# Kernel tuning notes

Hardware: AMD Instinct MI355X
Metric: run time of the kernel (lower is better)

## Reference

```python
import jax, jax.numpy as jnp
import numpy as np

B, N, IN_DIM, DIM = 16, 512, 2048, 512
K, DEPTH, HEADS, DH, MLP, NC = 4, 2, 8, 64, 512, 10
INNER = HEADS * DH  # 512
TOPK = 2
TEMP = 1.0


def setup_inputs() -> dict:
    key = jax.random.key(0)
    ks = jax.random.split(key, 16)
    g = lambda i, shape, s=0.02: jax.random.normal(ks[i], shape, dtype=jnp.float32) * s
    z = lambda shape: jnp.zeros(shape, jnp.float32)
    o = lambda shape: jnp.ones(shape, jnp.float32)
    return {
        "x": jax.random.normal(ks[0], (B, N, IN_DIM), dtype=jnp.float32),
        "proj_w": g(1, (IN_DIM, DIM)),
        "proj_b": z((DIM,)),
        "qkv_w": g(2, (K, DEPTH, DIM, 3 * INNER)),
        "ao_w": g(3, (K, DEPTH, INNER, DIM)),
        "ao_b": z((K, DEPTH, DIM)),
        "ln1_g": o((K, DEPTH, DIM)),
        "ln1_b": z((K, DEPTH, DIM)),
        "ln2_g": o((K, DEPTH, DIM)),
        "ln2_b": z((K, DEPTH, DIM)),
        "mlp_w1": g(4, (K, DEPTH, DIM, MLP)),
        "mlp_b1": z((K, DEPTH, MLP)),
        "mlp_w2": g(5, (K, DEPTH, MLP, DIM)),
        "mlp_b2": z((K, DEPTH, DIM)),
        "lnf_g": o((K, DIM)),
        "lnf_b": z((K, DIM)),
        "router_w1": g(6, (DIM, 256)),
        "router_b1": z((256,)),
        "router_w2": g(7, (256, K)),
        "router_b2": z((K,)),
        "head_w1": g(8, (DIM, 128)),
        "head_b1": z((128,)),
        "head_w2": g(9, (128, NC)),
        "head_b2": z((NC,)),
    }


def _ln(x, g, b):
    m = x.mean(-1, keepdims=True)
    v = jnp.mean((x - m) ** 2, axis=-1, keepdims=True)
    return (x - m) * jax.lax.rsqrt(v + 1e-5) * g + b


def _expert(h, qkv_w, ao_w, ao_b, ln1g, ln1b, ln2g, ln2b, w1, b1, w2, b2, lnfg, lnfb):
    # h: [B, N, DIM]; pre-norm transformer, depth=DEPTH, then final LN + mean-pool.
    Bb, Nn, _ = h.shape
    scale = DH ** -0.5
    for l in range(DEPTH):
        y = _ln(h, ln1g[l], ln1b[l])
        q, k, v = jnp.split(y @ qkv_w[l], 3, axis=-1)
        q = q.reshape(Bb, Nn, HEADS, DH)
        k = k.reshape(Bb, Nn, HEADS, DH)
        v = v.reshape(Bb, Nn, HEADS, DH)
        att = jax.nn.softmax(jnp.einsum('bqhd,bkhd->bhqk', q, k) * scale, axis=-1)
        o = jnp.einsum('bhqk,bkhd->bqhd', att, v).reshape(Bb, Nn, INNER)
        h = h + o @ ao_w[l] + ao_b[l]
        y2 = _ln(h, ln2g[l], ln2b[l])
        h = h + jax.nn.gelu(y2 @ w1[l] + b1[l]) @ w2[l] + b2[l]
    return _ln(h, lnfg, lnfb).mean(1)  # [B, DIM]


def reference(x, proj_w, proj_b, qkv_w, ao_w, ao_b, ln1_g, ln1_b, ln2_g, ln2_b,
              mlp_w1, mlp_b1, mlp_w2, mlp_b2, lnf_g, lnf_b,
              router_w1, router_b1, router_w2, router_b2,
              head_w1, head_b1, head_w2, head_b2):
    # Shared projection (mode='shared')
    H = x @ proj_w + proj_b                       # [B, N, DIM]
    bag = H.mean(1)                               # [B, DIM]
    rl = jax.nn.relu(bag @ router_w1 + router_b1) @ router_w2 + router_b2
    g_soft = jax.nn.softmax(rl / TEMP, axis=-1)   # [B, K]
    vals, idx = jax.lax.top_k(g_soft, TOPK)
    w = vals / (vals.sum(-1, keepdims=True) + 1e-8)
    # Dense combine weights: [B, K], zero for non-selected experts.
    Wfull = (jax.nn.one_hot(idx, K, dtype=H.dtype) * w[..., None]).sum(1)
    latents = jnp.stack([
        _expert(H, qkv_w[e], ao_w[e], ao_b[e], ln1_g[e], ln1_b[e], ln2_g[e], ln2_b[e],
                mlp_w1[e], mlp_b1[e], mlp_w2[e], mlp_b2[e], lnf_g[e], lnf_b[e])
        for e in range(K)
    ])                                            # [K, B, DIM]
    z = jnp.einsum('kbd,bk->bd', latents, Wfull)  # weighted combine
    logits = jax.nn.relu(z @ head_w1 + head_b1) @ head_w2 + head_b2
    return (z, logits, g_soft)
```

## Files before the change

kernel.cpp:

```cpp
#include <hip/hip_runtime.h>
#include <math.h>

typedef unsigned short u16;
typedef unsigned int u32;
typedef float f32x4 __attribute__((ext_vector_type(4)));
typedef unsigned short u16x8 __attribute__((ext_vector_type(8)));
typedef unsigned short u16x4 __attribute__((ext_vector_type(4)));
typedef _Float16 f16x8 __attribute__((ext_vector_type(8)));

#define DEV static __device__ __forceinline__

constexpr int BB = 16, NN = 512, DIM = 512, DEP = 2;
constexpr long ROWS = (long)BB * NN;

DEV u16 f2h(float f){ _Float16 h = (_Float16)f; return __builtin_bit_cast(u16, h); }
DEV float h2f(u16 u){ return (float)__builtin_bit_cast(_Float16, u); }
DEV f32x4 mfma16h(u16x8 a, u16x8 b, f32x4 c){
  return __builtin_amdgcn_mfma_f32_16x16x32_f16(__builtin_bit_cast(f16x8, a), __builtin_bit_cast(f16x8, b), c, 0, 0, 0);
}
DEV u32 pkrtz(float a, float b){ auto r = __builtin_amdgcn_cvt_pkrtz(a, b); return __builtin_bit_cast(u32, r); }
DEV float gelu_f(float x){ return 0.5f * x * (1.f + tanhf(0.79788456080286536f * (x + 0.044715f * x * x * x))); }

DEV void gload16(const u16* g, u16* l){
  __builtin_amdgcn_global_load_lds((const __attribute__((address_space(1))) unsigned int*)(const void*)g,
                                   (__attribute__((address_space(3))) unsigned int*)(void*)l, 16, 0, 0);
}

DEV f32x4 vaddv(f32x4 a, f32x4 b){ f32x4 r; r[0]=a[0]+b[0]; r[1]=a[1]+b[1]; r[2]=a[2]+b[2]; r[3]=a[3]+b[3]; return r; }
DEV f32x4 shfl4(f32x4 v, int m){ f32x4 r; r[0]=__shfl_xor(v[0],m); r[1]=__shfl_xor(v[1],m); r[2]=__shfl_xor(v[2],m); r[3]=__shfl_xor(v[3],m); return r; }

__global__ __launch_bounds__(256) void castAll(const float* __restrict__ qkv_w, const float* __restrict__ ao_w,
                                               const float* __restrict__ mlp_w1, const float* __restrict__ mlp_w2,
                                               u16* __restrict__ WQ, u16* __restrict__ WAO,
                                               u16* __restrict__ W1t, u16* __restrict__ W2t)
{
  const int z = blockIdx.z;
  const float* src; u16* dst; int Nd;
  if (z < 8){ src = qkv_w + (long)z * 512 * 1536; dst = WQ + (long)z * 512 * 1536; Nd = 1536; }
  else {
    int m = (z - 8) >> 3, zz = (z - 8) & 7;
    src = (m == 0 ? ao_w : m == 1 ? mlp_w1 : mlp_w2) + (long)zz * 512 * 512;
    dst = (m == 0 ? WAO : m == 1 ? W1t : W2t) + (long)zz * 512 * 512;
    Nd = 512;
  }
  const int n0 = blockIdx.y * 32;
  if (n0 >= Nd) return;
  const int k0 = blockIdx.x * 32;
  __shared__ float t[32][33];
  const int r = threadIdx.x >> 5, cc = threadIdx.x & 31;
  #pragma unroll
  for (int i = 0; i < 4; i++) t[r + i * 8][cc] = src[(long)(k0 + r + i * 8) * Nd + n0 + cc];
  __syncthreads();
  #pragma unroll
  for (int i = 0; i < 4; i++) dst[(long)(n0 + r + i * 8) * 512 + k0 + cc] = f2h(t[cc][r + i * 8]);
}

__global__ __launch_bounds__(256) void castTp(const float* __restrict__ src, u16* __restrict__ dst)
{
  __shared__ float t[32][33];
  const int k0 = blockIdx.x * 32, n0 = blockIdx.y * 32;
  const int r = threadIdx.x >> 5, cc = threadIdx.x & 31;
  #pragma unroll
  for (int i = 0; i < 4; i++) t[r + i * 8][cc] = src[(long)(k0 + r + i * 8) * 512 + n0 + cc];
  __syncthreads();
  #pragma unroll
  for (int i = 0; i < 4; i++) dst[(long)(n0 + r + i * 8) * 2048 + k0 + cc] = f2h(t[cc][r + i * 8]);
}

__global__ __launch_bounds__(256) void xcast(const float* __restrict__ X, u16* __restrict__ Xf)
{
  long i0 = ((long)blockIdx.x * 256 + threadIdx.x) * 8;
  f32x4 v0 = *(const f32x4*)(X + i0), v1 = *(const f32x4*)(X + i0 + 4);
  u16x8 hh;
  hh[0] = f2h(v0[0]); hh[1] = f2h(v0[1]); hh[2] = f2h(v0[2]); hh[3] = f2h(v0[3]);
  hh[4] = f2h(v1[0]); hh[5] = f2h(v1[1]); hh[6] = f2h(v1[2]); hh[7] = f2h(v1[3]);
  *(u16x8*)(Xf + i0) = hh;
}

__global__ __launch_bounds__(256) void gemm_proj(const u16* __restrict__ Xf, const u16* __restrict__ WP,
                                                 const float* __restrict__ bias, u16* __restrict__ Hout)
{
  const int mt = blockIdx.x, nt = blockIdx.y;
  __shared__ __align__(16) u16 As[64 * 64], Bs[128 * 64];
  const int tid = threadIdx.x, lane = tid & 63, wv = tid >> 6;
  const int wm = wv >> 1, wn = wv & 1, l4 = lane >> 4, l15 = lane & 15;
  const long a0 = (long)(mt * 64) * 2048, b0 = (long)(nt * 128) * 2048;
  const int srow = tid >> 3, sslot = tid & 7;
  f32x4 zero = {0.f, 0.f, 0.f, 0.f};
  f32x4 acc[2][4];
  #pragma unroll
  for (int mi = 0; mi < 2; mi++)
    #pragma unroll
    for (int ni = 0; ni < 4; ni++) acc[mi][ni] = zero;

  for (int kt = 0; kt < 2048; kt += 64){
    #pragma unroll
    for (int p = 0; p < 2; p++){
      int r = p * 32 + srow;
      int sg = sslot ^ (r & 7);
      gload16(Xf + a0 + (long)r * 2048 + kt + sg * 8, As + p * 2048 + wv * 512);
    }
    #pragma unroll
    for (int p = 0; p < 4; p++){
      int r = p * 32 + srow;
      int sg = sslot ^ (r & 7);
      gload16(WP + b0 + (long)r * 2048 + kt + sg * 8, Bs + p * 2048 + wv * 512);
    }
    __syncthreads();
    #pragma unroll
    for (int ks = 0; ks < 2; ks++){
      u16x8 af[2], bfr[4];
      #pragma unroll
      for (int mi = 0; mi < 2; mi++){
        int ra = wm * 32 + mi * 16 + l15;
        af[mi] = *(const u16x8*)(As + ra * 64 + ((((ks << 2) | l4)) ^ (ra & 7)) * 8);
      }
      #pragma unroll
      for (int ni = 0; ni < 4; ni++){
        int rb = wn * 64 + ni * 16 + l15;
        bfr[ni] = *(const u16x8*)(Bs + rb * 64 + ((((ks << 2) | l4)) ^ (rb & 7)) * 8);
      }
      #pragma unroll
      for (int mi = 0; mi < 2; mi++)
        #pragma unroll
        for (int ni = 0; ni < 4; ni++)
          acc[mi][ni] = mfma16h(af[mi], bfr[ni], acc[mi][ni]);
    }
    __syncthreads();
  }
  #pragma unroll
  for (int mi = 0; mi < 2; mi++)
    #pragma unroll
    for (int ni = 0; ni < 4; ni++){
      const int gr0 = mt * 64 + wm * 32 + mi * 16 + l4 * 4;
      const int gc = nt * 128 + wn * 64 + ni * 16 + l15;
      float bb = bias[gc];
      #pragma unroll
      for (int i = 0; i < 4; i++) Hout[(long)(gr0 + i) * 512 + gc] = f2h(acc[mi][ni][i] + bb);
    }
}

template<int EPI>
__global__ __launch_bounds__(256) void gemm_bt(const u16* __restrict__ A, int K, long sAe,
                                               const u16* __restrict__ Bt, long sBe,
                                               const float* __restrict__ bias, int sBiasE,
                                               u16* __restrict__ Cout, long sCe, int N,
                                               const int* __restrict__ pairs,
                                               const u16* __restrict__ resin)
{
  const int pe = pairs[blockIdx.x >> 2];
  const int e = pe >> 4, bb = pe & 15;
  const int row0 = bb * 512 + (blockIdx.x & 3) * 128;
  const int nt = blockIdx.y;
  A += (long)e * sAe + (long)row0 * K;
  Bt += (long)e * sBe + (long)(nt * 128) * K;
  const float* bias_e = bias ? bias + (long)e * sBiasE : nullptr;

  __shared__ __align__(16) u16 As[128 * 64];
  __shared__ __align__(16) u16 Bs[128 * 64];
  const int tid = threadIdx.x, lane = tid & 63, wv = tid >> 6;
  const int wm = wv >> 1, wn = wv & 1, l4 = lane >> 4, l15 = lane & 15;
  const int srow = tid >> 3, sslot = tid & 7;
  f32x4 zero = {0.f, 0.f, 0.f, 0.f};
  f32x4 acc[4][4];
  #pragma unroll
  for (int mi = 0; mi < 4; mi++)
    #pragma unroll
    for (int ni = 0; ni < 4; ni++) acc[mi][ni] = zero;

  for (int kt = 0; kt < K; kt += 64){
    #pragma unroll
    for (int p = 0; p < 4; p++){
      int r = p * 32 + srow;
      int sg = sslot ^ (r & 7);
      long go = (long)r * K + kt + sg * 8;
      int lo = p * 2048 + wv * 512;
      gload16(A + go, As + lo);
      gload16(Bt + go, Bs + lo);
    }
    __syncthreads();
    #pragma unroll
    for (int ks = 0; ks < 2; ks++){
      u16x8 af[4], bfr[4];
      #pragma unroll
      for (int mi = 0; mi < 4; mi++){
        int ra = wm * 64 + mi * 16 + l15;
        af[mi] = *(const u16x8*)(As + ra * 64 + ((((ks << 2) | l4)) ^ (ra & 7)) * 8);
      }
      #pragma unroll
      for (int ni = 0; ni < 4; ni++){
        int rb = wn * 64 + ni * 16 + l15;
        bfr[ni] = *(const u16x8*)(Bs + rb * 64 + ((((ks << 2) | l4)) ^ (rb & 7)) * 8);
      }
      #pragma unroll
      for (int mi = 0; mi < 4; mi++)
        #pragma unroll
        for (int ni = 0; ni < 4; ni++)
          acc[mi][ni] = mfma16h(af[mi], bfr[ni], acc[mi][ni]);
    }
    __syncthreads();
  }

  #pragma unroll
  for (int mi = 0; mi < 4; mi++)
    #pragma unroll
    for (int ni = 0; ni < 4; ni++){
      const int gr0 = row0 + wm * 64 + mi * 16 + l4 * 4;
      const int gc = nt * 128 + wn * 64 + ni * 16 + l15;
      float bb2 = bias_e ? bias_e[gc] : 0.f;
      #pragma unroll
      for (int i = 0; i < 4; i++){
        float val = acc[mi][ni][i] + bb2;
        long idx = (long)e * sCe + (long)(gr0 + i) * N + gc;
        if (EPI == 0){
          Cout[idx] = f2h(val);
        } else if (EPI == 1){
          Cout[idx] = f2h(gelu_f(val));
        } else if (EPI == 2){
          Cout[idx] = f2h(h2f(Cout[idx]) + val);
        } else {
          Cout[idx] = f2h(h2f(resin[(long)(gr0 + i) * N + gc]) + val);
        }
      }
    }
}

__global__ __launch_bounds__(256) void attn(const u16* __restrict__ qkv, u16* __restrict__ obf, const int* __restrict__ pairs)
{
  const int pe = pairs[blockIdx.x >> 5];
  const int e = pe >> 4, b = pe & 15;
  const int r5 = blockIdx.x & 31;
  const int hh = r5 >> 2, qt = r5 & 3;
  const u16* base = qkv + ((long)e * ROWS + (long)b * NN) * 1536;

  __shared__ u16 Ks[64 * 72];
  __shared__ u16 Vts[64 * 72];
  __shared__ u16 Ps[4][32 * 72];
  __shared__ float Lq[4][32];
  const int tid = threadIdx.x, lane = tid & 63, wv = tid >> 6;
  const int l4 = lane >> 4, l15 = lane & 15;
  const int qr0 = qt * 128 + wv * 32;
  constexpr float CSC = 0.125f * 1.44269504088896340736f;

  u16x8 qf[2][2];
  #pragma unroll
  for (int mi = 0; mi < 2; mi++)
    #pragma unroll
    for (int ks = 0; ks < 2; ks++){
      u16x8 raw = *(const u16x8*)(base + (long)(qr0 + mi * 16 + l15) * 1536 + hh * 64 + ks * 32 + l4 * 8);
      #pragma unroll
      for (int j = 0; j < 8; j++) qf[mi][ks][j] = f2h(h2f(raw[j]) * CSC);
    }

  f32x4 zero = {0.f, 0.f, 0.f, 0.f};
  f32x4 o[2][4]; float lrun[2] = {0.f, 0.f};
  #pragma unroll
  for (int mi = 0; mi < 2; mi++)
    #pragma unroll
    for (int df = 0; df < 4; df++) o[mi][df] = zero;
  const int sr = tid >> 3, ss = tid & 7;

  for (int c = 0; c < 8; c++){
    const int kk0 = c * 64;
    u16x8 kv0 = *(const u16x8*)(base + (long)(kk0 + sr) * 1536 + 512 + hh * 64 + ss * 8);
    u16x8 kv1 = *(const u16x8*)(base + (long)(kk0 + sr + 32) * 1536 + 512 + hh * 64 + ss * 8);
    u16x8 vv0 = *(const u16x8*)(base + (long)(kk0 + sr) * 1536 + 1024 + hh * 64 + ss * 8);
    u16x8 vv1 = *(const u16x8*)(base + (long)(kk0 + sr + 32) * 1536 + 1024 + hh * 64 + ss * 8);
    __syncthreads();
    *(u16x8*)(Ks + sr * 72 + ss * 8) = kv0;
    *(u16x8*)(Ks + (sr + 32) * 72 + ss * 8) = kv1;
    #pragma unroll
    for (int j = 0; j < 8; j++){
      Vts[(ss * 8 + j) * 72 + sr] = vv0[j];
      Vts[(ss * 8 + j) * 72 + sr + 32] = vv1[j];
    }
    __syncthreads();

    u16x8 kf[4][2];
    #pragma unroll
    for (int n = 0; n < 4; n++)
      #pragma unroll
      for (int ks = 0; ks < 2; ks++)
        kf[n][ks] = *(const u16x8*)(Ks + (n * 16 + l15) * 72 + ks * 32 + l4 * 8);

    f32x4 sv[2][4];
    #pragma unroll
    for (int mi = 0; mi < 2; mi++)
      #pragma unroll
      for (int n = 0; n < 4; n++){
        sv[mi][n] = zero;
        sv[mi][n] = mfma16h(kf[n][0], qf[mi][0], sv[mi][n]);
        sv[mi][n] = mfma16h(kf[n][1], qf[mi][1], sv[mi][n]);
      }

    #pragma unroll
    for (int mi = 0; mi < 2; mi++){
      float lp = 0.f;
      #pragma unroll
      for (int n = 0; n < 4; n++){
        float p0 = __builtin_amdgcn_exp2f(sv[mi][n][0]);
        float p1 = __builtin_amdgcn_exp2f(sv[mi][n][1]);
        float p2 = __builtin_amdgcn_exp2f(sv[mi][n][2]);
        float p3 = __builtin_amdgcn_exp2f(sv[mi][n][3]);
        lp += (p0 + p1) + (p2 + p3);
        union { u32 w[2]; u16x4 h; } pk;
        pk.w[0] = pkrtz(p0, p1);
        pk.w[1] = pkrtz(p2, p3);
        *(u16x4*)(&Ps[wv][(mi * 16 + l15) * 72 + n * 16 + l4 * 4]) = pk.h;
      }
      lp += __shfl_xor(lp, 16);
      lp += __shfl_xor(lp, 32);
      lrun[mi] += lp;
    }

    u16x8 pf[2][2], vf[4][2];
    #pragma unroll
    for (int mi = 0; mi < 2; mi++)
      #pragma unroll
      for (int k2 = 0; k2 < 2; k2++)
        pf[mi][k2] = *(const u16x8*)(&Ps[wv][(mi * 16 + l15) * 72 + k2 * 32 + l4 * 8]);
    #pragma unroll
    for (int df = 0; df < 4; df++)
      #pragma unroll
      for (int k2 = 0; k2 < 2; k2++)
        vf[df][k2] = *(const u16x8*)(Vts + (df * 16 + l15) * 72 + k2 * 32 + l4 * 8);
    #pragma unroll
    for (int mi = 0; mi < 2; mi++)
      #pragma unroll
      for (int df = 0; df < 4; df++){
        o[mi][df] = mfma16h(pf[mi][0], vf[df][0], o[mi][df]);
        o[mi][df] = mfma16h(pf[mi][1], vf[df][1], o[mi][df]);
      }
  }

  if (l4 == 0){
    Lq[wv][l15] = lrun[0];
    Lq[wv][16 + l15] = lrun[1];
  }
  __syncthreads();
  #pragma unroll
  for (int mi = 0; mi < 2; mi++){
    f32x4 inv;
    #pragma unroll
    for (int i = 0; i < 4; i++) inv[i] = 1.f / Lq[wv][mi * 16 + l4 * 4 + i];
    #pragma unroll
    for (int df = 0; df < 4; df++)
      #pragma unroll
      for (int i = 0; i < 4; i++)
        obf[(long)e * ROWS * DIM + (long)(b * NN + qr0 + mi * 16 + l4 * 4 + i) * DIM + hh * 64 + df * 16 + l15]
          = f2h(o[mi][df][i] * inv[i]);
  }
}

__global__ __launch_bounds__(256) void ln_rows(const u16* __restrict__ hin, long sHe,
                                               const float* __restrict__ g, const float* __restrict__ bta,
                                               int sGE, u16* __restrict__ outb, const int* __restrict__ pairs)
{
  const int pe = pairs[blockIdx.x >> 9];
  const int e = pe >> 4;
  const int row = (pe & 15) * 512 + (blockIdx.x & 511);
  const u16* x = hin + (long)e * sHe + (long)row * DIM;
  const int tid = threadIdx.x, lane = tid & 63, wv = tid >> 6;
  float a0 = h2f(x[tid]), a1 = h2f(x[tid + 256]);
  float s = a0 + a1, sq = a0 * a0 + a1 * a1;
  #pragma unroll
  for (int m = 32; m >= 1; m >>= 1){ s += __shfl_xor(s, m); sq += __shfl_xor(sq, m); }
  __shared__ float red[2][4];
  if (lane == 0){ red[0][wv] = s; red[1][wv] = sq; }
  __syncthreads();
  float S = red[0][0] + red[0][1] + red[0][2] + red[0][3];
  float Q = red[1][0] + red[1][1] + red[1][2] + red[1][3];
  float mean = S * (1.f / DIM); float var = Q * (1.f / DIM) - mean * mean;
  float inv = rsqrtf(var + 1e-5f);
  const float* ge = g + (long)e * sGE; const float* be = bta + (long)e * sGE;
  u16* yo = outb + ((long)e * ROWS + row) * DIM;
  yo[tid] = f2h((a0 - mean) * inv * ge[tid] + be[tid]);
  yo[tid + 256] = f2h((a1 - mean) * inv * ge[tid + 256] + be[tid + 256]);
}

__global__ __launch_bounds__(512) void bag_partial(const u16* __restrict__ H, float* __restrict__ bagp)
{
  const int b = blockIdx.x, c = blockIdx.y;
  const int tid = threadIdx.x;
  const u16* r = H + ((long)b * 512 + c * 64) * DIM + tid;
  float s = 0.f;
  #pragma unroll 8
  for (int n = 0; n < 64; n++) s += h2f(r[n * DIM]);
  bagp[((long)c * BB + b) * DIM + tid] = s;
}

__global__ __launch_bounds__(256) void router_mm(const float* __restrict__ bagp, const float* __restrict__ rw1,
                                                 float* __restrict__ hidp)
{
  const int kc = blockIdx.x, b = blockIdx.y;
  const int tid = threadIdx.x;
  __shared__ float bs[64];
  if (tid < 64){
    int k = kc * 64 + tid;
    float s = 0.f;
    #pragma unroll
    for (int c = 0; c < 8; c++) s += bagp[((long)c * BB + b) * DIM + k];
    bs[tid] = s * (1.f / NN);
  }
  __syncthreads();
  float a = 0.f;
  #pragma unroll 8
  for (int k = 0; k < 64; k++) a += bs[k] * rw1[(long)(kc * 64 + k) * 256 + tid];
  hidp[((long)b * 8 + kc) * 256 + tid] = a;
}

__global__ __launch_bounds__(256) void router_fin(const float* __restrict__ hidp,
                                                  const float* __restrict__ rb1,
                                                  const float* __restrict__ rw2, const float* __restrict__ rb2,
                                                  float* __restrict__ gout, float* __restrict__ wexp, int* __restrict__ pairs)
{
  const int b = blockIdx.x;
  const int tid = threadIdx.x, lane = tid & 63, wv = tid >> 6;
  __shared__ f32x4 red2[4];
  float a = rb1[tid];
  #pragma unroll
  for (int kc = 0; kc < 8; kc++) a += hidp[((long)b * 8 + kc) * 256 + tid];
  float h = fmaxf(a, 0.f);
  f32x4 w4 = *(const f32x4*)(rw2 + tid * 4);
  f32x4 s = {h * w4[0], h * w4[1], h * w4[2], h * w4[3]};
  s = vaddv(s, shfl4(s, 1)); s = vaddv(s, shfl4(s, 2)); s = vaddv(s, shfl4(s, 4));
  s = vaddv(s, shfl4(s, 8)); s = vaddv(s, shfl4(s, 16)); s = vaddv(s, shfl4(s, 32));
  if (lane == 0) red2[wv] = s;
  __syncthreads();
  if (tid == 0){
    f32x4 lg = vaddv(vaddv(red2[0], red2[1]), vaddv(red2[2], red2[3]));
    float l4a[4]; float m = -3e38f;
    #pragma unroll
    for (int k = 0; k < 4; k++){ l4a[k] = lg[k] + rb2[k]; m = fmaxf(m, l4a[k]); }
    float ex[4]; float ssum2 = 0;
    #pragma unroll
    for (int k = 0; k < 4; k++){ ex[k] = expf(l4a[k] - m); ssum2 += ex[k]; }
    float gv[4];
    #pragma unroll
    for (int k = 0; k < 4; k++){ gv[k] = ex[k] / ssum2; gout[b * 4 + k] = gv[k]; }
    int i0 = 0; float v0 = gv[0];
    #pragma unroll
    for (int k = 1; k < 4; k++) if (gv[k] > v0){ v0 = gv[k]; i0 = k; }
    int i1 = -1; float v1 = -1.f;
    #pragma unroll
    for (int k = 0; k < 4; k++) if (k != i0 && gv[k] > v1){ v1 = gv[k]; i1 = k; }
    float den = v0 + v1 + 1e-8f;
    #pragma unroll
    for (int k = 0; k < 4; k++) wexp[k * BB + b] = (k == i0) ? (v0 / den) : ((k == i1) ? (v1 / den) : 0.f);
    pairs[2 * b]     = (i0 << 4) | b;
    pairs[2 * b + 1] = (i1 << 4) | b;
  }
}

__global__ __launch_bounds__(512) void lnf_pool(const u16* __restrict__ hin, const float* __restrict__ g, const float* __restrict__ bta,
                                                float* __restrict__ latents, const int* __restrict__ pairs)
{
  const int pe = pairs[blockIdx.x];
  const int e = pe >> 4, b = pe & 15;
  const int tid = threadIdx.x, lane = tid & 63, wv = tid >> 6;
  __shared__ float gs[512], bsh[512];
  gs[tid] = g[e * DIM + tid]; bsh[tid] = bta[e * DIM + tid];
  __syncthreads();
  float acc[8] = {0, 0, 0, 0, 0, 0, 0, 0};
  for (int n = wv; n < NN; n += 8){
    const u16* r = hin + ((long)e * ROWS + (long)b * NN + n) * DIM + lane * 8;
    u16x8 vh = *(const u16x8*)r;
    float v[8];
    #pragma unroll
    for (int j = 0; j < 8; j++) v[j] = h2f(vh[j]);
    float s = 0, sq = 0;
    #pragma unroll
    for (int j = 0; j < 8; j++){ s += v[j]; sq += v[j] * v[j]; }
    #pragma unroll
    for (int m = 32; m >= 1; m >>= 1){ s += __shfl_xor(s, m); sq += __shfl_xor(sq, m); }
    float mean = s * (1.f / DIM), var = sq * (1.f / DIM) - mean * mean, inv = rsqrtf(var + 1e-5f);
    #pragma unroll
    for (int j = 0; j < 8; j++) acc[j] += (v[j] - mean) * inv * gs[lane * 8 + j] + bsh[lane * 8 + j];
  }
  __shared__ float red[8][512];
  #pragma unroll
  for (int j = 0; j < 8; j++) red[wv][lane * 8 + j] = acc[j];
  __syncthreads();
  float ssum = 0;
  #pragma unroll
  for (int w = 0; w < 8; w++) ssum += red[w][tid];
  latents[((long)e * BB + b) * DIM + tid] = ssum * (1.f / NN);
}

__global__ __launch_bounds__(128) void combine_head(const float* __restrict__ latents, const float* __restrict__ wexp,
                                                    const float* __restrict__ hw1, const float* __restrict__ hb1,
                                                    const float* __restrict__ hw2, const float* __restrict__ hb2,
                                                    float* __restrict__ out)
{
  const int b = blockIdx.x;
  const int tid = threadIdx.x;
  __shared__ float zs[512];
  __shared__ float hid[128];
  float wk[4];
  #pragma unroll
  for (int k = 0; k < 4; k++) wk[k] = wexp[k * BB + b];
  #pragma unroll
  for (int i = 0; i < 4; i++){
    int c = tid + i * 128;
    float s = 0.f;
    #pragma unroll
    for (int k = 0; k < 4; k++) if (wk[k] != 0.f) s += wk[k] * latents[((long)k * BB + b) * DIM + c];
    zs[c] = s; out[b * 512 + c] = s;
  }
  __syncthreads();
  float h = hb1[tid];
  #pragma unroll 8
  for (int k2 = 0; k2 < 512; k2++) h += zs[k2] * hw1[k2 * 128 + tid];
  hid[tid] = fmaxf(h, 0.f);
  __syncthreads();
  if (tid < 10){
    float s = hb2[tid];
    #pragma unroll 16
    for (int j = 0; j < 128; j++) s += hid[j] * hw2[j * 10 + tid];
    out[8192 + b * 10 + tid] = s;
  }
}

extern "C" void kernel_launch(void* const* d_in, const int* in_sizes, int n_in,
                              void* d_out, int out_size, void* d_ws, size_t ws_size,
                              hipStream_t stream)
{
  const float* x      = (const float*)d_in[0];
  const float* proj_w = (const float*)d_in[1];
  const float* proj_b = (const float*)d_in[2];
  const float* qkv_w  = (const float*)d_in[3];
  const float* ao_w   = (const float*)d_in[4];
  const float* ao_b   = (const float*)d_in[5];
  const float* ln1_g  = (const float*)d_in[6];
  const float* ln1_b  = (const float*)d_in[7];
  const float* ln2_g  = (const float*)d_in[8];
  const float* ln2_b  = (const float*)d_in[9];
  const float* mlp_w1 = (const float*)d_in[10];
  const float* mlp_b1 = (const float*)d_in[11];
  const float* mlp_w2 = (const float*)d_in[12];
  const float* mlp_b2 = (const float*)d_in[13];
  const float* lnf_g  = (const float*)d_in[14];
  const float* lnf_b  = (const float*)d_in[15];
  const float* rw1    = (const float*)d_in[16];
  const float* rb1    = (const float*)d_in[17];
  const float* rw2    = (const float*)d_in[18];
  const float* rb2    = (const float*)d_in[19];
  const float* hw1    = (const float*)d_in[20];
  const float* hb1    = (const float*)d_in[21];
  const float* hw2    = (const float*)d_in[22];
  const float* hb2    = (const float*)d_in[23];
  float* out = (float*)d_out;

  char* base = (char*)d_ws; size_t off = 0;
  auto alloc = [&](size_t bytes) -> void* { void* p = base + off; off = (off + bytes + 255) & ~(size_t)255; return p; };

  u16* WQ   = (u16*)alloc((size_t)8 * 1536 * 512 * 2);
  u16* WAO  = (u16*)alloc((size_t)8 * 512 * 512 * 2);
  u16* W1t  = (u16*)alloc((size_t)8 * 512 * 512 * 2);
  u16* W2t  = (u16*)alloc((size_t)8 * 512 * 512 * 2);
  u16* WP   = (u16*)alloc((size_t)512 * 2048 * 2);
  u16* HF   = (u16*)alloc((size_t)ROWS * 512 * 2);
  u16* HH   = (u16*)alloc((size_t)4 * ROWS * 512 * 2);
  u16* YB   = (u16*)alloc((size_t)4 * ROWS * 512 * 2);
  u16* QKVb = (u16*)alloc((size_t)4 * ROWS * 1536 * 2);
  float* WEXP = (float*)alloc(64 * 4);
  int* PAIRS  = (int*)alloc(32 * 4);
  float* LAT  = (float*)alloc(4 * 16 * 512 * 4);
  float* BAGP = (float*)alloc((size_t)8 * 16 * 512 * 4);
  float* HIDP = (float*)alloc((size_t)16 * 8 * 256 * 4);
  u16* Y2B = QKVb;
  u16* TB  = QKVb + (size_t)4 * ROWS * 512;
  u16* OB  = YB;
  u16* Xf  = QKVb;

  castAll<<<dim3(16, 48, 32), 256, 0, stream>>>(qkv_w, ao_w, mlp_w1, mlp_w2, WQ, WAO, W1t, W2t);
  castTp<<<dim3(64, 16), 256, 0, stream>>>(proj_w, WP);
  xcast<<<8192, 256, 0, stream>>>(x, Xf);

  gemm_proj<<<dim3(128, 4), 256, 0, stream>>>(Xf, WP, proj_b, HF);
  bag_partial<<<dim3(16, 8), 512, 0, stream>>>(HF, BAGP);
  router_mm<<<dim3(8, 16), 256, 0, stream>>>(BAGP, rw1, HIDP);
  router_fin<<<16, 256, 0, stream>>>(HIDP, rb1, rw2, rb2, out + 8192 + 160, WEXP, PAIRS);

  for (int l = 0; l < 2; l++){
    if (l == 0)
      ln_rows<<<16384, 256, 0, stream>>>(HF, 0L, ln1_g, ln1_b, DEP * 512, YB, PAIRS);
    else
      ln_rows<<<16384, 256, 0, stream>>>(HH, ROWS * 512, ln1_g + 512, ln1_b + 512, DEP * 512, YB, PAIRS);
    gemm_bt<0><<<dim3(128, 12), 256, 0, stream>>>(YB, 512, ROWS * 512, WQ + (long)l * 1536 * 512, (long)DEP * 1536 * 512,
                                                  nullptr, 0, QKVb, ROWS * 1536, 1536, PAIRS, nullptr);
    attn<<<1024, 256, 0, stream>>>(QKVb, OB, PAIRS);
    if (l == 0)
      gemm_bt<3><<<dim3(128, 4), 256, 0, stream>>>(OB, 512, ROWS * 512, WAO, (long)DEP * 512 * 512,
                                                   ao_b, DEP * 512, HH, ROWS * 512, 512, PAIRS, HF);
    else
      gemm_bt<2><<<dim3(128, 4), 256, 0, stream>>>(OB, 512, ROWS * 512, WAO + (long)512 * 512, (long)DEP * 512 * 512,
                                                   ao_b + 512, DEP * 512, HH, ROWS * 512, 512, PAIRS, nullptr);
    ln_rows<<<16384, 256, 0, stream>>>(HH, ROWS * 512, ln2_g + l * 512, ln2_b + l * 512, DEP * 512, Y2B, PAIRS);
    gemm_bt<1><<<dim3(128, 4), 256, 0, stream>>>(Y2B, 512, ROWS * 512, W1t + (long)l * 512 * 512, (long)DEP * 512 * 512,
                                                 mlp_b1 + l * 512, DEP * 512, TB, ROWS * 512, 512, PAIRS, nullptr);
    gemm_bt<2><<<dim3(128, 4), 256, 0, stream>>>(TB, 512, ROWS * 512, W2t + (long)l * 512 * 512, (long)DEP * 512 * 512,
                                                 mlp_b2 + l * 512, DEP * 512, HH, ROWS * 512, 512, PAIRS, nullptr);
  }

  lnf_pool<<<32, 512, 0, stream>>>(HH, lnf_g, lnf_b, LAT, PAIRS);
  combine_head<<<16, 128, 0, stream>>>(LAT, WEXP, hw1, hb1, hw2, hb2, out);
}
```

Baseline: 515.9 us.

## Swizzle attention V tile, reorder attn grid, set MFMA priority, warp-per-row LayerNorm

The attention kernel now XOR-swizzles the transposed V tile in shared memory to reduce bank conflicts on the scalar transpose stores. It reorders the block index so consecutive blocks cover different (expert,batch) pairs rather than heads of the same pair, and raises wave priority around the MFMA sections. LayerNorm is rewritten as one wavefront per row with 16-byte vector loads and stores and no shared-memory reduction or barrier, launching a quarter as many blocks. The swizzle must match exactly between writes and reads, and the new block ordering changes L2 locality for K/V reuse.

Result: faster. 478.0 us (-7.3%).

```diff
diff --git a/kernel.cpp b/kernel.cpp
--- a/kernel.cpp
+++ b/kernel.cpp
@@ -227,10 +227,10 @@
 
 __global__ __launch_bounds__(256) void attn(const u16* __restrict__ qkv, u16* __restrict__ obf, const int* __restrict__ pairs)
 {
-  const int pe = pairs[blockIdx.x >> 5];
+  const int pe = pairs[blockIdx.x & 31];
   const int e = pe >> 4, b = pe & 15;
-  const int r5 = blockIdx.x & 31;
-  const int hh = r5 >> 2, qt = r5 & 3;
+  const int hh = (blockIdx.x >> 5) & 7;
+  const int qt = blockIdx.x >> 8;
   const u16* base = qkv + ((long)e * ROWS + (long)b * NN) * 1536;
 
   __shared__ u16 Ks[64 * 72];
@@ -271,8 +271,9 @@
     *(u16x8*)(Ks + (sr + 32) * 72 + ss * 8) = kv1;
     #pragma unroll
     for (int j = 0; j < 8; j++){
-      Vts[(ss * 8 + j) * 72 + sr] = vv0[j];
-      Vts[(ss * 8 + j) * 72 + sr + 32] = vv1[j];
+      int d = ss * 8 + j;
+      Vts[d * 72 + (sr ^ (ss * 8))] = vv0[j];
+      Vts[d * 72 + ((sr + 32) ^ (ss * 8))] = vv1[j];
     }
     __syncthreads();
 
@@ -284,6 +285,7 @@
         kf[n][ks] = *(const u16x8*)(Ks + (n * 16 + l15) * 72 + ks * 32 + l4 * 8);
 
     f32x4 sv[2][4];
+    __builtin_amdgcn_s_setprio(1);
     #pragma unroll
     for (int mi = 0; mi < 2; mi++)
       #pragma unroll
@@ -292,6 +294,7 @@
         sv[mi][n] = mfma16h(kf[n][0], qf[mi][0], sv[mi][n]);
         sv[mi][n] = mfma16h(kf[n][1], qf[mi][1], sv[mi][n]);
       }
+    __builtin_amdgcn_s_setprio(0);
 
     #pragma unroll
     for (int mi = 0; mi < 2; mi++){
@@ -322,8 +325,12 @@
     #pragma unroll
     for (int df = 0; df < 4; df++)
       #pragma unroll
-      for (int k2 = 0; k2 < 2; k2++)
-        vf[df][k2] = *(const u16x8*)(Vts + (df * 16 + l15) * 72 + k2 * 32 + l4 * 8);
+      for (int k2 = 0; k2 < 2; k2++){
+        int d = df * 16 + l15;
+        int swz = ((d >> 3) & 7) * 8;
+        vf[df][k2] = *(const u16x8*)(Vts + d * 72 + ((k2 * 32 + l4 * 8) ^ swz));
+      }
+    __builtin_amdgcn_s_setprio(1);
     #pragma unroll
     for (int mi = 0; mi < 2; mi++)
       #pragma unroll
@@ -331,6 +338,7 @@
         o[mi][df] = mfma16h(pf[mi][0], vf[df][0], o[mi][df]);
         o[mi][df] = mfma16h(pf[mi][1], vf[df][1], o[mi][df]);
       }
+    __builtin_amdgcn_s_setprio(0);
   }
 
   if (l4 == 0){
@@ -356,26 +364,32 @@
                                                const float* __restrict__ g, const float* __restrict__ bta,
                                                int sGE, u16* __restrict__ outb, const int* __restrict__ pairs)
 {
-  const int pe = pairs[blockIdx.x >> 9];
+  const int pe = pairs[blockIdx.x >> 7];
   const int e = pe >> 4;
-  const int row = (pe & 15) * 512 + (blockIdx.x & 511);
-  const u16* x = hin + (long)e * sHe + (long)row * DIM;
   const int tid = threadIdx.x, lane = tid & 63, wv = tid >> 6;
-  float a0 = h2f(x[tid]), a1 = h2f(x[tid + 256]);
-  float s = a0 + a1, sq = a0 * a0 + a1 * a1;
+  const int row = (pe & 15) * 512 + ((blockIdx.x & 127) << 2) + wv;
+  const u16* x = hin + (long)e * sHe + (long)row * DIM + lane * 8;
+  u16x8 vh = *(const u16x8*)x;
+  float v[8];
+  #pragma unroll
+  for (int j = 0; j < 8; j++) v[j] = h2f(vh[j]);
+  float s = 0.f, sq = 0.f;
+  #pragma unroll
+  for (int j = 0; j < 8; j++){ s += v[j]; sq += v[j] * v[j]; }
   #pragma unroll
   for (int m = 32; m >= 1; m >>= 1){ s += __shfl_xor(s, m); sq += __shfl_xor(sq, m); }
-  __shared__ float red[2][4];
-  if (lane == 0){ red[0][wv] = s; red[1][wv] = sq; }
-  __syncthreads();
-  float S = red[0][0] + red[0][1] + red[0][2] + red[0][3];
-  float Q = red[1][0] + red[1][1] + red[1][2] + red[1][3];
-  float mean = S * (1.f / DIM); float var = Q * (1.f / DIM) - mean * mean;
+  float mean = s * (1.f / DIM); float var = sq * (1.f / DIM) - mean * mean;
   float inv = rsqrtf(var + 1e-5f);
-  const float* ge = g + (long)e * sGE; const float* be = bta + (long)e * sGE;
-  u16* yo = outb + ((long)e * ROWS + row) * DIM;
-  yo[tid] = f2h((a0 - mean) * inv * ge[tid] + be[tid]);
-  yo[tid + 256] = f2h((a1 - mean) * inv * ge[tid + 256] + be[tid + 256]);
+  const float* ge = g + (long)e * sGE + lane * 8;
+  const float* be = bta + (long)e * sGE + lane * 8;
+  f32x4 g0 = *(const f32x4*)ge, g1 = *(const f32x4*)(ge + 4);
+  f32x4 b0 = *(const f32x4*)be, b1 = *(const f32x4*)(be + 4);
+  u16x8 yo;
+  #pragma unroll
+  for (int j = 0; j < 4; j++) yo[j] = f2h((v[j] - mean) * inv * g0[j] + b0[j]);
+  #pragma unroll
+  for (int j = 0; j < 4; j++) yo[4 + j] = f2h((v[4 + j] - mean) * inv * g1[j] + b1[j]);
+  *(u16x8*)(outb + ((long)e * ROWS + row) * DIM + lane * 8) = yo;
 }
 
 __global__ __launch_bounds__(512) void bag_partial(const u16* __restrict__ H, float* __restrict__ bagp)
@@ -584,9 +598,9 @@
 
   for (int l = 0; l < 2; l++){
     if (l == 0)
-      ln_rows<<<16384, 256, 0, stream>>>(HF, 0L, ln1_g, ln1_b, DEP * 512, YB, PAIRS);
+      ln_rows<<<4096, 256, 0, stream>>>(HF, 0L, ln1_g, ln1_b, DEP * 512, YB, PAIRS);
     else
-      ln_rows<<<16384, 256, 0, stream>>>(HH, ROWS * 512, ln1_g + 512, ln1_b + 512, DEP * 512, YB, PAIRS);
+      ln_rows<<<4096, 256, 0, stream>>>(HH, ROWS * 512, ln1_g + 512, ln1_b + 512, DEP * 512, YB, PAIRS);
     gemm_bt<0><<<dim3(128, 12), 256, 0, stream>>>(YB, 512, ROWS * 512, WQ + (long)l * 1536 * 512, (long)DEP * 1536 * 512,
                                                   nullptr, 0, QKVb, ROWS * 1536, 1536, PAIRS, nullptr);
     attn<<<1024, 256, 0, stream>>>(QKVb, OB, PAIRS);
@@ -596,7 +610,7 @@
     else
       gemm_bt<2><<<dim3(128, 4), 256, 0, stream>>>(OB, 512, ROWS * 512, WAO + (long)512 * 512, (long)DEP * 512 * 512,
                                                    ao_b + 512, DEP * 512, HH, ROWS * 512, 512, PAIRS, nullptr);
-    ln_rows<<<16384, 256, 0, stream>>>(HH, ROWS * 512, ln2_g + l * 512, ln2_b + l * 512, DEP * 512, Y2B, PAIRS);
+    ln_rows<<<4096, 256, 0, stream>>>(HH, ROWS * 512, ln2_g + l * 512, ln2_b + l * 512, DEP * 512, Y2B, PAIRS);
     gemm_bt<1><<<dim3(128, 4), 256, 0, stream>>>(Y2B, 512, ROWS * 512, W1t + (long)l * 512 * 512, (long)DEP * 512 * 512,
                                                  mlp_b1 + l * 512, DEP * 512, TB, ROWS * 512, 512, PAIRS, nullptr);
     gemm_bt<2><<<dim3(128, 4), 256, 0, stream>>>(TB, 512, ROWS * 512, W2t + (long)l * 512 * 512, (long)DEP * 512 * 512,
```
